# Optimization experiments

Hardware: AMD Instinct MI355X
Metric: run time of the kernel (lower is better)

The kernel has to match this reference:

```python
import jax, jax.numpy as jnp
import numpy as np

EMBED_DIM = 64


def _knn_graph(dist, k):
    """dist: [n, n]. Returns src [n,k], nbr [n,k], d [n,k] with self-edges removed,
    neighbors in ascending-distance order (matches torch.topk largest=False + self filter)."""
    n = dist.shape[0]
    _, idx = jax.lax.top_k(-dist, k + 1)  # [n, k+1] indices, ascending distance
    node = jnp.arange(n)[:, None]
    # stable reorder pushing the self index to the end, preserving distance order
    key = jnp.arange(k + 1)[None, :] + (k + 2) * (idx == node)
    order = jnp.argsort(key, axis=-1)
    nbr = jnp.take_along_axis(idx, order, axis=-1)[:, :k]  # [n, k]
    d = jnp.take_along_axis(dist, nbr, axis=-1)            # [n, k]
    src = jnp.broadcast_to(node, (n, k))
    return src, nbr, d


def setup_inputs() -> dict:
    key = jax.random.key(0)
    k1, k2, k3, k4 = jax.random.split(key, 4)
    B, n = 8, 1000
    locs = jax.random.uniform(k1, (B, n, 2), dtype=jnp.float32)
    init_embeddings = jax.random.normal(k2, (B, n, EMBED_DIM), dtype=jnp.float32)
    # nn.Linear(1, embed_dim): W [embed_dim, 1], b [embed_dim]
    W = jax.random.normal(k3, (EMBED_DIM, 1), dtype=jnp.float32)
    b = jax.random.normal(k4, (EMBED_DIM,), dtype=jnp.float32)
    return {"locs": locs, "init_embeddings": init_embeddings, "W": W, "b": b, "k_sparse": 200}


def reference(locs, init_embeddings, W, b, k_sparse):
    B, n, _ = locs.shape
    # cdist p=2: [B, n, n]
    diff = locs[:, :, None, :] - locs[:, None, :, :]
    dist = jnp.sqrt(jnp.sum(diff * diff, axis=-1))
    src, nbr, d = jax.vmap(lambda dm: _knn_graph(dm, k_sparse))(dist)  # [B, n, k]
    # Batch.from_data_list: concatenate graphs with node-index offsets
    off = (jnp.arange(B, dtype=src.dtype) * n)[:, None, None]
    edge_index = jnp.stack([(src + off).reshape(-1), (nbr + off).reshape(-1)], axis=0)  # [2, B*n*k]
    x = init_embeddings.reshape(B * n, -1)  # batch.x
    edge_attr = d.reshape(-1, 1)            # [E, 1]
    edge_emb = edge_attr @ W.T + b          # [E, embed_dim]
    return x, edge_index.astype(jnp.int32), edge_emb
```

## Files before the change

kernel.cpp:

```cpp
#include <hip/hip_runtime.h>
#include <stdint.h>

#define NNODE 1000
#define KSP   200
#define DIM   64
#define BATCH 8
#define WPB   8
#define NBLK  (BATCH * NNODE / WPB)

__global__ __launch_bounds__(512) void knn_edge_kernel(
    const float* __restrict__ locs,
    const float* __restrict__ emb,
    const float* __restrict__ W,
    const float* __restrict__ bias,
    float* __restrict__ out)
{
    __shared__ float4   sloc4[NNODE / 2];
    __shared__ int      hist[WPB][256];
    __shared__ uint64_t cand[WPB][256];
    __shared__ int      ssp[WPB];

    const int tid  = threadIdx.x;
    const int w    = tid >> 6;
    const int lane = tid & 63;
    const int node = blockIdx.x * WPB + w;
    const int b    = node / NNODE;
    const int i    = node - b * NNODE;

    if (tid < NNODE / 2) sloc4[tid] = ((const float4*)(locs + (size_t)b * NNODE * 2))[tid];
    ((int4*)hist)[tid] = make_int4(0, 0, 0, 0);
    if (tid < WPB) ssp[tid] = KSP + 1;
    __syncthreads();

    const float2* sloc = (const float2*)sloc4;
    const float2 self = sloc[i];

    const size_t E = (size_t)BATCH * NNODE * KSP;
    float* x_out = out;
    float* ei0   = out + (size_t)BATCH * NNODE * DIM;
    float* ei1   = ei0 + E;
    float* eemb  = ei1 + E;

    const int c4 = (lane & 15) << 2;
    const float4 w4 = *(const float4*)(W + c4);
    const float4 b4 = *(const float4*)(bias + c4);

    x_out[(size_t)node * DIM + lane] = emb[(size_t)node * DIM + lane];
    const size_t ebase = (size_t)node * KSP;
    const float fnode = (float)node;
    for (int t = lane; t < KSP; t += 64) ei0[ebase + t] = fnode;

    for (int j = lane; j < NNODE; j += 64) {
        float2 pt = sloc[j];
        float dx = __fsub_rn(self.x, pt.x);
        float dy = __fsub_rn(self.y, pt.y);
        float d  = __fsqrt_rn(__fadd_rn(__fmul_rn(dx, dx), __fmul_rn(dy, dy)));
        int q = (int)(d * 180.0f);
        q = q > 255 ? 255 : q;
        atomicAdd(&hist[w][q], 1);
    }
    __builtin_amdgcn_wave_barrier();

    int4 h4 = ((int4*)&hist[w][0])[lane];
    int s0 = h4.x;
    int s1 = s0 + h4.y;
    int s2 = s1 + h4.z;
    int s3 = s2 + h4.w;
    int sc = s3;
    #pragma unroll
    for (int off = 1; off < 64; off <<= 1) {
        int y = __shfl_up(sc, off, 64);
        if (lane >= off) sc += y;
    }
    const int excl = sc - s3;
    int bc = 1 << 30;
    if      (excl + s0 >= KSP + 1) bc = 4 * lane;
    else if (excl + s1 >= KSP + 1) bc = 4 * lane + 1;
    else if (excl + s2 >= KSP + 1) bc = 4 * lane + 2;
    else if (excl + s3 >= KSP + 1) bc = 4 * lane + 3;
    #pragma unroll
    for (int off = 32; off; off >>= 1) bc = min(bc, __shfl_xor(bc, off, 64));
    const int B = bc;
    int4 st;
    st.x = excl;
    st.y = excl + s0;
    st.z = excl + s1;
    st.w = excl + s2;
    ((int4*)&hist[w][0])[lane] = st;
    __builtin_amdgcn_wave_barrier();

    for (int j = lane; j < NNODE; j += 64) {
        float2 pt = sloc[j];
        float dx = __fsub_rn(self.x, pt.x);
        float dy = __fsub_rn(self.y, pt.y);
        float d  = __fsqrt_rn(__fadd_rn(__fmul_rn(dx, dx), __fmul_rn(dy, dy)));
        int q = (int)(d * 180.0f);
        q = q > 255 ? 255 : q;
        if (q <= B) {
            int slot = atomicAdd(&hist[w][q], 1);
            if (slot < 256)
                cand[w][slot] = ((uint64_t)__float_as_uint(d) << 32) | (uint32_t)j;
        }
    }
    __builtin_amdgcn_wave_barrier();

    const int cumB = min(hist[w][B], 256);

    uint64_t mykey[4];
    int      myrank[4];
    #pragma unroll
    for (int s = 0; s < 4; ++s) {
        int t = lane + s * 64;
        myrank[s] = KSP + 1;
        if (t < cumB) {
            uint64_t k = cand[w][t];
            float d = __uint_as_float((uint32_t)(k >> 32));
            int q = (int)(d * 180.0f);
            q = q > 255 ? 255 : q;
            int start = q ? hist[w][q - 1] : 0;
            int end   = min(hist[w][q], 256);
            int r = start;
            for (int m = start; m < end; ++m)
                r += (cand[w][m] < k) ? 1 : 0;
            mykey[s]  = k;
            myrank[s] = r;
        }
    }
    __builtin_amdgcn_wave_barrier();

    #pragma unroll
    for (int s = 0; s < 4; ++s) {
        int t = lane + s * 64;
        if (t < cumB) {
            int r = myrank[s];
            if (r <= KSP) cand[w][r] = mykey[s];
            if ((uint32_t)mykey[s] == (uint32_t)i) ssp[w] = r;
        }
    }
    __builtin_amdgcn_wave_barrier();
    const int sp = ssp[w];

    for (int t = lane; t < KSP; t += 64) {
        int slot = t + (t >= sp ? 1 : 0);
        uint64_t kk = cand[w][slot];
        ei1[ebase + t] = (float)(b * NNODE + (int)(uint32_t)kk);
    }

    float4* em4 = (float4*)(eemb + ebase * DIM);
    for (int t = lane; t < KSP * (DIM / 4); t += 64) {
        int e    = t >> 4;
        int slot = e + (e >= sp ? 1 : 0);
        float d = __uint_as_float((uint32_t)(cand[w][slot] >> 32));
        float4 v;
        v.x = fmaf(d, w4.x, b4.x);
        v.y = fmaf(d, w4.y, b4.y);
        v.z = fmaf(d, w4.z, b4.z);
        v.w = fmaf(d, w4.w, b4.w);
        em4[t] = v;
    }
}

extern "C" void kernel_launch(void* const* d_in, const int* in_sizes, int n_in,
                              void* d_out, int out_size, void* d_ws, size_t ws_size,
                              hipStream_t stream) {
    const float* locs = (const float*)d_in[0];
    const float* emb  = (const float*)d_in[1];
    const float* W    = (const float*)d_in[2];
    const float* bias = (const float*)d_in[3];
    float* out = (float*)d_out;

    knn_edge_kernel<<<NBLK, 512, 0, stream>>>(locs, emb, W, bias, out);
}
```

Measured before the change: 93.38 us.

## Pipeline per-node KNN selection across waves with cooperative histogram passes

```diff
diff --git a/kernel.cpp b/kernel.cpp
--- a/kernel.cpp
+++ b/kernel.cpp
@@ -1,12 +1,13 @@
 #include <hip/hip_runtime.h>
 #include <stdint.h>
 
-#define NNODE 1000
-#define KSP   200
-#define DIM   64
-#define BATCH 8
-#define WPB   8
-#define NBLK  (BATCH * NNODE / WPB)
+#define NNODE  1000
+#define KSP    200
+#define DIM    64
+#define BATCH  8
+#define NPB    8
+#define NBLK   (BATCH * NNODE / NPB)
+#define NCHUNK 16
 
 __global__ __launch_bounds__(512) void knn_edge_kernel(
     const float* __restrict__ locs,
@@ -15,25 +16,28 @@
     const float* __restrict__ bias,
     float* __restrict__ out)
 {
-    __shared__ float4   sloc4[NNODE / 2];
-    __shared__ int      hist[WPB][256];
-    __shared__ uint64_t cand[WPB][256];
-    __shared__ int      ssp[WPB];
-
-    const int tid  = threadIdx.x;
-    const int w    = tid >> 6;
-    const int lane = tid & 63;
-    const int node = blockIdx.x * WPB + w;
-    const int b    = node / NNODE;
-    const int i    = node - b * NNODE;
-
-    if (tid < NNODE / 2) sloc4[tid] = ((const float4*)(locs + (size_t)b * NNODE * 2))[tid];
+    __shared__ float4         sloc4[NNODE / 2];
+    __shared__ int            hist[NPB][256];
+    __shared__ float          dS[NPB][256];
+    __shared__ unsigned short iS[NPB][256];
+    __shared__ float          stD[NPB][KSP];
+    __shared__ unsigned short stI[NPB][KSP];
+    __shared__ int            done1[NPB], done2[NPB], sB[NPB];
+
+    const int tid   = threadIdx.x;
+    const int wv    = tid >> 6;
+    const int lane  = tid & 63;
+    const int node0 = blockIdx.x * NPB;
+    const int b     = node0 / NNODE;
+    const int ibase = node0 - b * NNODE;
+
     ((int4*)hist)[tid] = make_int4(0, 0, 0, 0);
-    if (tid < WPB) ssp[tid] = KSP + 1;
+    if (tid < NPB) { done1[tid] = 0; done2[tid] = 0; sB[tid] = -1; }
+    if (tid < NNODE / 2)
+        sloc4[tid] = ((const float4*)(locs + (size_t)b * NNODE * 2))[tid];
     __syncthreads();
 
     const float2* sloc = (const float2*)sloc4;
-    const float2 self = sloc[i];
 
     const size_t E = (size_t)BATCH * NNODE * KSP;
     float* x_out = out;
@@ -45,118 +49,146 @@
     const float4 w4 = *(const float4*)(W + c4);
     const float4 b4 = *(const float4*)(bias + c4);
 
-    x_out[(size_t)node * DIM + lane] = emb[(size_t)node * DIM + lane];
-    const size_t ebase = (size_t)node * KSP;
-    const float fnode = (float)node;
-    for (int t = lane; t < KSP; t += 64) ei0[ebase + t] = fnode;
-
-    for (int j = lane; j < NNODE; j += 64) {
-        float2 pt = sloc[j];
-        float dx = __fsub_rn(self.x, pt.x);
-        float dy = __fsub_rn(self.y, pt.y);
-        float d  = __fsqrt_rn(__fadd_rn(__fmul_rn(dx, dx), __fmul_rn(dy, dy)));
-        int q = (int)(d * 180.0f);
-        q = q > 255 ? 255 : q;
-        atomicAdd(&hist[w][q], 1);
+    {
+        const int mynode = node0 + wv;
+        x_out[(size_t)mynode * DIM + lane] = emb[(size_t)mynode * DIM + lane];
+        const size_t eb = (size_t)mynode * KSP;
+        const float fn = (float)mynode;
+        for (int t = lane; t < KSP; t += 64) ei0[eb + t] = fn;
     }
-    __builtin_amdgcn_wave_barrier();
-
-    int4 h4 = ((int4*)&hist[w][0])[lane];
-    int s0 = h4.x;
-    int s1 = s0 + h4.y;
-    int s2 = s1 + h4.z;
-    int s3 = s2 + h4.w;
-    int sc = s3;
-    #pragma unroll
-    for (int off = 1; off < 64; off <<= 1) {
-        int y = __shfl_up(sc, off, 64);
-        if (lane >= off) sc += y;
-    }
-    const int excl = sc - s3;
-    int bc = 1 << 30;
-    if      (excl + s0 >= KSP + 1) bc = 4 * lane;
-    else if (excl + s1 >= KSP + 1) bc = 4 * lane + 1;
-    else if (excl + s2 >= KSP + 1) bc = 4 * lane + 2;
-    else if (excl + s3 >= KSP + 1) bc = 4 * lane + 3;
-    #pragma unroll
-    for (int off = 32; off; off >>= 1) bc = min(bc, __shfl_xor(bc, off, 64));
-    const int B = bc;
-    int4 st;
-    st.x = excl;
-    st.y = excl + s0;
-    st.z = excl + s1;
-    st.w = excl + s2;
-    ((int4*)&hist[w][0])[lane] = st;
-    __builtin_amdgcn_wave_barrier();
-
-    for (int j = lane; j < NNODE; j += 64) {
-        float2 pt = sloc[j];
-        float dx = __fsub_rn(self.x, pt.x);
-        float dy = __fsub_rn(self.y, pt.y);
-        float d  = __fsqrt_rn(__fadd_rn(__fmul_rn(dx, dx), __fmul_rn(dy, dy)));
-        int q = (int)(d * 180.0f);
-        q = q > 255 ? 255 : q;
-        if (q <= B) {
-            int slot = atomicAdd(&hist[w][q], 1);
-            if (slot < 256)
-                cand[w][slot] = ((uint64_t)__float_as_uint(d) << 32) | (uint32_t)j;
-        }
-    }
-    __builtin_amdgcn_wave_barrier();
-
-    const int cumB = min(hist[w][B], 256);
-
-    uint64_t mykey[4];
-    int      myrank[4];
-    #pragma unroll
-    for (int s = 0; s < 4; ++s) {
-        int t = lane + s * 64;
-        myrank[s] = KSP + 1;
-        if (t < cumB) {
-            uint64_t k = cand[w][t];
-            float d = __uint_as_float((uint32_t)(k >> 32));
-            int q = (int)(d * 180.0f);
-            q = q > 255 ? 255 : q;
-            int start = q ? hist[w][q - 1] : 0;
-            int end   = min(hist[w][q], 256);
-            int r = start;
-            for (int m = start; m < end; ++m)
-                r += (cand[w][m] < k) ? 1 : 0;
-            mykey[s]  = k;
-            myrank[s] = r;
-        }
-    }
-    __builtin_amdgcn_wave_barrier();
-
-    #pragma unroll
-    for (int s = 0; s < 4; ++s) {
-        int t = lane + s * 64;
-        if (t < cumB) {
-            int r = myrank[s];
-            if (r <= KSP) cand[w][r] = mykey[s];
-            if ((uint32_t)mykey[s] == (uint32_t)i) ssp[w] = r;
-        }
-    }
-    __builtin_amdgcn_wave_barrier();
-    const int sp = ssp[w];
-
-    for (int t = lane; t < KSP; t += 64) {
-        int slot = t + (t >= sp ? 1 : 0);
-        uint64_t kk = cand[w][slot];
-        ei1[ebase + t] = (float)(b * NNODE + (int)(uint32_t)kk);
-    }
-
-    float4* em4 = (float4*)(eemb + ebase * DIM);
-    for (int t = lane; t < KSP * (DIM / 4); t += 64) {
-        int e    = t >> 4;
-        int slot = e + (e >= sp ? 1 : 0);
-        float d = __uint_as_float((uint32_t)(cand[w][slot] >> 32));
-        float4 v;
-        v.x = fmaf(d, w4.x, b4.x);
-        v.y = fmaf(d, w4.y, b4.y);
-        v.z = fmaf(d, w4.z, b4.z);
-        v.w = fmaf(d, w4.w, b4.w);
-        em4[t] = v;
+
+    for (int k = 0; k < NPB; ++k) {
+        const int excused = (k + NPB - 1) & 7;
+        if (wv == excused) continue;
+
+        const int i_k = ibase + k;
+        const float2 self = sloc[i_k];
+        const int tIdx = (wv - k) & 7;
+
+        #pragma unroll
+        for (int cs = 0; cs < 3; ++cs) {
+            int c = cs * 7 + tIdx;
+            if (c < NCHUNK) {
+                int j = c * 64 + lane;
+                if (j < NNODE) {
+                    float2 pt = sloc[j];
+                    float dx = __fsub_rn(self.x, pt.x);
+                    float dy = __fsub_rn(self.y, pt.y);
+                    float d  = __fsqrt_rn(__fadd_rn(__fmul_rn(dx, dx), __fmul_rn(dy, dy)));
+                    int q = (int)(d * 180.0f);
+                    atomicAdd(&hist[k][q], 1);
+                }
+            }
+        }
+        if (lane == 0)
+            __hip_atomic_fetch_add(&done1[k], 1, __ATOMIC_RELEASE, __HIP_MEMORY_SCOPE_WORKGROUP);
+
+        if (wv == ((k + 1) & 7)) {
+            while (__hip_atomic_load(&done1[k], __ATOMIC_ACQUIRE, __HIP_MEMORY_SCOPE_WORKGROUP) < 7)
+                __builtin_amdgcn_s_sleep(1);
+            int4 h4 = ((int4*)&hist[k][0])[lane];
+            int s0 = h4.x, s1 = s0 + h4.y, s2 = s1 + h4.z, s3 = s2 + h4.w;
+            int sc = s3;
+            #pragma unroll
+            for (int off = 1; off < 64; off <<= 1) {
+                int y = __shfl_up(sc, off, 64);
+                if (lane >= off) sc += y;
+            }
+            int excl = sc - s3;
+            int bc = 1 << 30;
+            if      (excl + s0 >= KSP + 1) bc = 4 * lane;
+            else if (excl + s1 >= KSP + 1) bc = 4 * lane + 1;
+            else if (excl + s2 >= KSP + 1) bc = 4 * lane + 2;
+            else if (excl + s3 >= KSP + 1) bc = 4 * lane + 3;
+            #pragma unroll
+            for (int off = 32; off; off >>= 1) bc = min(bc, __shfl_xor(bc, off, 64));
+            int4 st;
+            st.x = excl; st.y = excl + s0; st.z = excl + s1; st.w = excl + s2;
+            ((int4*)&hist[k][0])[lane] = st;
+            __builtin_amdgcn_wave_barrier();
+            if (lane == 0)
+                __hip_atomic_store(&sB[k], bc, __ATOMIC_RELEASE, __HIP_MEMORY_SCOPE_WORKGROUP);
+        }
+        int Bk;
+        while ((Bk = __hip_atomic_load(&sB[k], __ATOMIC_ACQUIRE, __HIP_MEMORY_SCOPE_WORKGROUP)) < 0)
+            __builtin_amdgcn_s_sleep(1);
+
+        #pragma unroll
+        for (int cs = 0; cs < 3; ++cs) {
+            int c = cs * 7 + tIdx;
+            if (c < NCHUNK) {
+                int j = c * 64 + lane;
+                if (j < NNODE) {
+                    float2 pt = sloc[j];
+                    float dx = __fsub_rn(self.x, pt.x);
+                    float dy = __fsub_rn(self.y, pt.y);
+                    float d  = __fsqrt_rn(__fadd_rn(__fmul_rn(dx, dx), __fmul_rn(dy, dy)));
+                    int q = (int)(d * 180.0f);
+                    if (q <= Bk) {
+                        int slot = atomicAdd(&hist[k][q], 1);
+                        if (slot < 256) { dS[k][slot] = d; iS[k][slot] = (unsigned short)j; }
+                    }
+                }
+            }
+        }
+        if (lane == 0)
+            __hip_atomic_fetch_add(&done2[k], 1, __ATOMIC_RELEASE, __HIP_MEMORY_SCOPE_WORKGROUP);
+
+        if (wv == k) {
+            while (__hip_atomic_load(&done2[k], __ATOMIC_ACQUIRE, __HIP_MEMORY_SCOPE_WORKGROUP) < 7)
+                __builtin_amdgcn_s_sleep(1);
+
+            const int cumB = min(hist[k][Bk], 256);
+            float myd[4]; int myidx[4]; int myr[4];
+            int selfr = 0x7fffffff;
+            #pragma unroll
+            for (int s = 0; s < 4; ++s) {
+                int t = lane + s * 64;
+                myr[s] = KSP + 1;
+                if (t < cumB) {
+                    float d = dS[k][t];
+                    int idx = iS[k][t];
+                    int q = (int)(d * 180.0f);
+                    int start = q ? hist[k][q - 1] : 0;
+                    int end   = min(hist[k][q], 256);
+                    int r = start;
+                    for (int m = start; m < end; ++m) {
+                        float dm = dS[k][m]; int im = iS[k][m];
+                        r += (dm < d || (dm == d && im < idx)) ? 1 : 0;
+                    }
+                    myd[s] = d; myidx[s] = idx; myr[s] = r;
+                    if (idx == i_k) selfr = r;
+                }
+            }
+            #pragma unroll
+            for (int off = 32; off; off >>= 1) selfr = min(selfr, __shfl_xor(selfr, off, 64));
+            const int sp = selfr;
+            #pragma unroll
+            for (int s = 0; s < 4; ++s) {
+                int r = myr[s];
+                if (r <= KSP && r != sp) {
+                    int tt = r - (r > sp ? 1 : 0);
+                    if (tt < KSP) { stD[k][tt] = myd[s]; stI[k][tt] = (unsigned short)myidx[s]; }
+                }
+            }
+            __builtin_amdgcn_wave_barrier();
+
+            const size_t eb = (size_t)(node0 + k) * KSP;
+            for (int t = lane; t < KSP; t += 64)
+                ei1[eb + t] = (float)(b * NNODE + (int)stI[k][t]);
+
+            float4* em4 = (float4*)(eemb + eb * DIM);
+            for (int t = lane; t < KSP * (DIM / 4); t += 64) {
+                int e = t >> 4;
+                float d = stD[k][e];
+                float4 v;
+                v.x = fmaf(d, w4.x, b4.x);
+                v.y = fmaf(d, w4.y, b4.y);
+                v.z = fmaf(d, w4.z, b4.z);
+                v.w = fmaf(d, w4.w, b4.w);
+                em4[t] = v;
+            }
+        }
     }
 }
 
```

Result: slower. 151.8 us (+62.6%).
